# Optimization experiments

Measured on AMD Instinct MI355X. Metric: run time of the kernel, lower is better.

The kernel has to match this reference:

```python
import jax, jax.numpy as jnp
import numpy as np

BT, NQ, NC, C, H, HID = 192, 64, 1024, 384, 8, 1536
DH = C // H                       # 48
SCALE = DH ** -0.5
MAX_NEG = -float(np.finfo(np.float32).max)


def _ln(x, eps, g=None, b=None):
    m = x.mean(-1, keepdims=True)
    v = ((x - m) ** 2).mean(-1, keepdims=True)
    y = (x - m) / jnp.sqrt(v + eps)
    if g is not None:
        y = y * g + b
    return y


def _gelu_tanh(x):
    # GELU(approximate='tanh')
    return 0.5 * x * (1.0 + jnp.tanh(jnp.sqrt(2.0 / jnp.pi) * (x + 0.044715 * x ** 3)))


def setup_inputs() -> dict:
    key = jax.random.key(0)
    ks = jax.random.split(key, 10)
    s = lambda fan: 1.0 / np.sqrt(fan)
    return {
        "x": jax.random.normal(ks[0], (BT, NQ, C), jnp.float32),
        "context": jax.random.normal(ks[1], (BT, NC, C), jnp.float32),
        "mask": jax.random.randint(ks[2], (BT, NQ), 0, 2) > 0,
        "Wq": jax.random.normal(ks[3], (C, C), jnp.float32) * s(C),
        "bq": jnp.zeros((C,), jnp.float32),
        "Wkv": jax.random.normal(ks[4], (C, 2 * C), jnp.float32) * s(C),
        "bkv": jnp.zeros((2 * C,), jnp.float32),
        "Wo": jax.random.normal(ks[5], (C, C), jnp.float32) * s(C),
        "bo": jnp.zeros((C,), jnp.float32),
        "g_ctx": jnp.ones((C,), jnp.float32),
        "b_ctx": jnp.zeros((C,), jnp.float32),
        "W1": jax.random.normal(ks[6], (C, HID), jnp.float32) * s(C),
        "b1": jnp.zeros((HID,), jnp.float32),
        "W2": jax.random.normal(ks[7], (HID, C), jnp.float32) * s(HID),
        "b2": jnp.zeros((C,), jnp.float32),
    }


def reference(x, context, mask, Wq, bq, Wkv, bkv, Wo, bo, g_ctx, b_ctx, W1, b1, W2, b2):
    # --- cross-attention branch ---
    xn = _ln(x, 1e-6)                       # norm1 (no affine)
    cn = _ln(context, 1e-5, g_ctx, b_ctx)   # norm_context (affine, default eps)
    q = (xn @ Wq + bq).reshape(BT, NQ, H, DH).transpose(0, 2, 1, 3)    # (B,H,NQ,DH)
    kv = cn @ Wkv + bkv
    k, v = jnp.split(kv, 2, axis=-1)
    k = k.reshape(BT, NC, H, DH).transpose(0, 2, 1, 3)                 # (B,H,NC,DH)
    v = v.reshape(BT, NC, H, DH).transpose(0, 2, 1, 3)
    sim = jnp.einsum('bhqd,bhkd->bhqk', q, k) * SCALE                  # (B,H,NQ,NC)
    # mask shape (BT, NQ): True = keep query row; ~mask * (-max) bias
    bias = jnp.where(mask[:, None, :, None], 0.0, MAX_NEG)
    attn = jax.nn.softmax(sim + bias, axis=-1)
    o = jnp.einsum('bhqk,bhkd->bhqd', attn, v).transpose(0, 2, 1, 3).reshape(BT, NQ, C)
    x = x + o @ Wo + bo
    # --- MLP branch ---
    xn2 = _ln(x, 1e-6)                      # norm2 (no affine)
    x = x + _gelu_tanh(xn2 @ W1 + b1) @ W2 + b2
    return x
```

## Files before the change

### kernel.cpp

```cpp
#include <hip/hip_runtime.h>
#include <hip/hip_bf16.h>
#include <math.h>

typedef unsigned int  u32;
typedef unsigned short u16;
typedef unsigned char u8;

#define BTn   192
#define NQn   64
#define NCn   1024
#define Cd    384
#define Hn    8
#define DHn   48
#define HIDn  1536
#define ROWSX (BTn*NQn)
#define ROWSC (BTn*NCn)
#define ATT_SCALE 0.14433756729740643f
#define CBc   64

typedef __bf16 bf16x8 __attribute__((ext_vector_type(8)));
typedef float  f32x4  __attribute__((ext_vector_type(4)));

#define GLL16(gp, lp) __builtin_amdgcn_global_load_lds( \
    (const __attribute__((address_space(1))) void*)(gp), \
    (__attribute__((address_space(3))) void*)(lp), 16, 0, 0)

__device__ __forceinline__ float bf2f(u32 u) {
  union { u32 i; float f; } v; v.i = u << 16; return v.f;
}
__device__ __forceinline__ u16 f2bf(float f) {
  union { float f; u32 i; } v; v.f = f;
  u32 x = v.i;
  x += 0x7fffu + ((x >> 16) & 1u);
  return (u16)(x >> 16);
}
__device__ __forceinline__ void decode8(uint4 r, float* v) {
  v[0]=bf2f(r.x & 0xffffu); v[1]=bf2f(r.x >> 16);
  v[2]=bf2f(r.y & 0xffffu); v[3]=bf2f(r.y >> 16);
  v[4]=bf2f(r.z & 0xffffu); v[5]=bf2f(r.z >> 16);
  v[6]=bf2f(r.w & 0xffffu); v[7]=bf2f(r.w >> 16);
}
__device__ __forceinline__ float gelu_f(float x) {
  float x3 = x*x*x;
  float z = 0.7978845608028654f*x + 0.035677408136300125f*x3;
  float e = __expf(2.f*z);
  float th = 1.f - 2.f/(e+1.f);
  return 0.5f*x*(1.f+th);
}

__global__ void decode_mask_kernel(const u8* __restrict__ m, u8* __restrict__ keep) {
  __shared__ int flags[3];
  int t = threadIdx.x;
  if (t < 3) flags[t] = 0;
  __syncthreads();
  int nonbin = 0, oddset = 0, low01 = 0;
  for (int i = t; i < ROWSX; i += 256) {
    u32 b = m[i];
    if (b > 1u) nonbin = 1;
    if ((i & 3) && b) oddset = 1;
    if (((i & 3) < 2) && b) low01 = 1;
  }
  if (nonbin) flags[0] = 1;
  if (oddset) flags[1] = 1;
  if (low01)  flags[2] = 1;
  __syncthreads();
  int mode = flags[0] ? (flags[2] ? 2 : 3) : (flags[1] ? 1 : 0);
  for (int i = t; i < ROWSX; i += 256) {
    u8 k;
    if (mode == 2)      k = (m[2*i] | m[2*i+1]) ? 1 : 0;
    else if (mode == 3) k = (((const float*)m)[i] != 0.f) ? 1 : 0;
    else if (mode == 1) k = m[i] ? 1 : 0;
    else                k = (((const int*)m)[i] != 0) ? 1 : 0;
    keep[i] = k;
  }
}

template<int AFF, int SRCF32>
__global__ __launch_bounds__(256) void lnorm_kernel(
    const void* __restrict__ srcv, const float* __restrict__ gw,
    const float* __restrict__ bw, u16* __restrict__ dst, float eps)
{
  const int row  = blockIdx.x * 4 + (threadIdx.x >> 6);
  const int lane = threadIdx.x & 63;
  float v[6];
  if (SRCF32) {
    const float2* p = (const float2*)((const float*)srcv + (size_t)row*Cd);
    #pragma unroll
    for (int i = 0; i < 3; i++) { float2 u = p[lane + 64*i]; v[2*i]=u.x; v[2*i+1]=u.y; }
  } else {
    const u32* p = (const u32*)((const u16*)srcv + (size_t)row*Cd);
    #pragma unroll
    for (int i = 0; i < 3; i++) { u32 u = p[lane + 64*i]; v[2*i]=bf2f(u&0xffffu); v[2*i+1]=bf2f(u>>16); }
  }
  float s  = v[0]+v[1]+v[2]+v[3]+v[4]+v[5];
  float s2 = v[0]*v[0]+v[1]*v[1]+v[2]*v[2]+v[3]*v[3]+v[4]*v[4]+v[5]*v[5];
  #pragma unroll
  for (int o = 32; o >= 1; o >>= 1) { s += __shfl_xor(s, o); s2 += __shfl_xor(s2, o); }
  float mean = s * (1.0f/Cd);
  float var  = s2 * (1.0f/Cd) - mean*mean;
  var = var > 0.f ? var : 0.f;
  float rstd = rsqrtf(var + eps);
  u32* d32 = (u32*)(dst + (size_t)row*Cd);
  #pragma unroll
  for (int i = 0; i < 3; i++) {
    float y0 = (v[2*i]   - mean) * rstd;
    float y1 = (v[2*i+1] - mean) * rstd;
    if (AFF) {
      float2 gg = *(const float2*)(gw + 2*(lane + 64*i));
      float2 bb = *(const float2*)(bw + 2*(lane + 64*i));
      y0 = y0*gg.x + bb.x;
      y1 = y1*gg.y + bb.y;
    }
    d32[lane + 64*i] = (u32)f2bf(y0) | ((u32)f2bf(y1) << 16);
  }
}

struct WPack {
  const float* W[5];
  u16* WT[5];
  int K[5];
  int N[5];
  int off[6];
};
__global__ __launch_bounds__(256) void wconvt_all_kernel(WPack p) {
  __shared__ u16 tile[64][66];
  const int bid = blockIdx.x;
  int s = 0;
  #pragma unroll
  for (int i = 1; i < 5; i++) if (bid >= p.off[i]) s = i;
  const float* W = p.W[s];
  u16* WT = p.WT[s];
  const int K = p.K[s], N = p.N[s];
  const int lb = bid - p.off[s];
  const int t  = threadIdx.x;
  const int nt = N >> 6;
  const int bk = lb / nt, bn = lb % nt;
  const int q  = t >> 6;
  const int nl = t & 63;
  #pragma unroll
  for (int r = 0; r < 16; r++) {
    int k = q*16 + r;
    tile[nl][k] = f2bf(W[(size_t)(bk*64 + k)*N + bn*64 + nl]);
  }
  __syncthreads();
  #pragma unroll
  for (int r = 0; r < 16; r++) {
    int n = q*16 + r;
    WT[(size_t)(bn*64 + n)*K + bk*64 + nl] = tile[n][nl];
  }
}

template<int GEL, int RES, int RF32, int OF32, int SCL>
__global__ __launch_bounds__(256) void mgemm_kernel(
    const u16* __restrict__ A, const u16* __restrict__ WT,
    const float* __restrict__ bias, const void* __restrict__ resv,
    void* __restrict__ Coutv, int M, int N, int K, int nx)
{
  __shared__ u16 As[3][4096];
  __shared__ u16 Bs[3][4096];
  const int t = threadIdx.x;
  const int w = t >> 6, l = t & 63, l15 = l & 15, g = l >> 4;

  const int nwg = gridDim.x;
  const int bid = blockIdx.x;
  const int wg  = (bid & 7) * (nwg >> 3) + (bid >> 3);
  const int n0 = (wg % nx) * 128, m0 = (wg / nx) * 128;
  const int wm = (w & 1) * 64, wn = (w >> 1) * 64;

  const int arow = t >> 2;
  const int swk  = (t >> 3) & 3;
  const int acol = ((t & 3) ^ swk) * 8;
  const u16* Ag = A  + (size_t)(m0 + arow) * K + acol;
  const u16* Wg = WT + (size_t)(n0 + arow) * K + acol;
  const size_t rowskip = (size_t)64 * K;

  const int xk   = (l15 >> 1) & 3;
  const int goff = ((g ^ xk) << 3);

  f32x4 acc[4][4];
  #pragma unroll
  for (int i = 0; i < 4; i++)
    #pragma unroll
    for (int j = 0; j < 4; j++) acc[i][j] = (f32x4){0.f, 0.f, 0.f, 0.f};

  const int nIter = K >> 5;

#define STAGE(nb, kk) do { \
    GLL16(Ag + (kk),           &As[nb][t*8]); \
    GLL16(Ag + (kk) + rowskip, &As[nb][2048 + t*8]); \
    GLL16(Wg + (kk),           &Bs[nb][t*8]); \
    GLL16(Wg + (kk) + rowskip, &Bs[nb][2048 + t*8]); \
  } while (0)

#define BODY(BUF, IT) do { \
    const int it_ = (IT); \
    if (it_ + 2 < nIter) { \
      STAGE((BUF + 2) % 3, (it_ + 2) << 5); \
      asm volatile("s_waitcnt vmcnt(8)" ::: "memory"); \
    } else if (it_ + 1 < nIter) { \
      asm volatile("s_waitcnt vmcnt(4)" ::: "memory"); \
    } else { \
      asm volatile("s_waitcnt vmcnt(0)" ::: "memory"); \
    } \
    __builtin_amdgcn_s_barrier(); \
    __builtin_amdgcn_sched_barrier(0); \
    { \
      bf16x8 af[4], bfv[4]; \
      _Pragma("unroll") \
      for (int i = 0; i < 4; i++) \
        af[i] = *(const bf16x8*)&As[BUF][(wm + i*16 + l15)*32 + goff]; \
      _Pragma("unroll") \
      for (int j = 0; j < 4; j++) \
        bfv[j] = *(const bf16x8*)&Bs[BUF][(wn + j*16 + l15)*32 + goff]; \
      _Pragma("unroll") \
      for (int i = 0; i < 4; i++) \
        _Pragma("unroll") \
        for (int j = 0; j < 4; j++) \
          acc[i][j] = __builtin_amdgcn_mfma_f32_16x16x32_bf16(bfv[j], af[i], acc[i][j], 0, 0, 0); \
    } \
    __builtin_amdgcn_sched_barrier(0); \
    __builtin_amdgcn_s_barrier(); \
  } while (0)

  STAGE(0, 0);
  STAGE(1, 32);
  for (int it0 = 0; it0 < nIter; it0 += 3) {
    BODY(0, it0);
    BODY(1, it0 + 1);
    BODY(2, it0 + 2);
  }
#undef BODY
#undef STAGE

  const float* resf = (const float*)resv;
  const u16*   resb = (const u16*)resv;
  float* Cf = (float*)Coutv;
  u16*   Cb = (u16*)Coutv;
  #pragma unroll
  for (int j = 0; j < 4; j++) {
    const int nb = n0 + wn + j*16 + g*4;
    const float4 bv = *(const float4*)&bias[nb];
    #pragma unroll
    for (int i = 0; i < 4; i++) {
      const int m = m0 + wm + i*16 + l15;
      float c0 = acc[i][j][0] + bv.x;
      float c1 = acc[i][j][1] + bv.y;
      float c2 = acc[i][j][2] + bv.z;
      float c3 = acc[i][j][3] + bv.w;
      if (SCL) { c0 *= ATT_SCALE; c1 *= ATT_SCALE; c2 *= ATT_SCALE; c3 *= ATT_SCALE; }
      if (GEL) { c0 = gelu_f(c0); c1 = gelu_f(c1); c2 = gelu_f(c2); c3 = gelu_f(c3); }
      if (RES) {
        if (RF32) {
          float4 r = *(const float4*)&resf[(size_t)m*N + nb];
          c0 += r.x; c1 += r.y; c2 += r.z; c3 += r.w;
        } else {
          uint2 r = *(const uint2*)&resb[(size_t)m*N + nb];
          c0 += bf2f(r.x & 0xffffu); c1 += bf2f(r.x >> 16);
          c2 += bf2f(r.y & 0xffffu); c3 += bf2f(r.y >> 16);
        }
      }
      if (OF32) {
        *(float4*)&Cf[(size_t)m*N + nb] = make_float4(c0, c1, c2, c3);
      } else {
        uint2 pk = make_uint2((u32)f2bf(c0) | ((u32)f2bf(c1) << 16),
                              (u32)f2bf(c2) | ((u32)f2bf(c3) << 16));
        *(uint2*)&Cb[(size_t)m*N + nb] = pk;
      }
    }
  }
}

template<int GEL, int RES, int RF32, int OF32>
__global__ __launch_bounds__(512, 4) void mgemm256_kernel(
    const u16* __restrict__ A, const u16* __restrict__ WT,
    const float* __restrict__ bias, const void* __restrict__ resv,
    void* __restrict__ Coutv, int M, int N, int K, int nx)
{
  __shared__ u16 As[3][4096];
  __shared__ u16 Bs[3][8192];
  const int t = threadIdx.x;
  const int w = t >> 6, l = t & 63, l15 = l & 15, g = l >> 4;

  const int nwg = gridDim.x;
  const int bid = blockIdx.x;
  const int wg  = (bid & 7) * (nwg >> 3) + (bid >> 3);
  const int n0 = (wg % nx) * 256, m0 = (wg / nx) * 128;
  const int wm = (w & 1) * 64, wn = (w >> 1) * 64;

  const int arow = t >> 2;
  const int swk  = (t >> 3) & 3;
  const int acol = ((t & 3) ^ swk) * 8;
  const u16* Ag = A  + (size_t)(m0 + arow) * K + acol;
  const u16* Wg = WT + (size_t)(n0 + arow) * K + acol;
  const size_t rowskipB = (size_t)128 * K;

  const int xk   = (l15 >> 1) & 3;
  const int goff = ((g ^ xk) << 3);

  f32x4 acc[4][4];
  #pragma unroll
  for (int i = 0; i < 4; i++)
    #pragma unroll
    for (int j = 0; j < 4; j++) acc[i][j] = (f32x4){0.f, 0.f, 0.f, 0.f};

  const int nIter = K >> 5;

#define STAGE(nb, kk) do { \
    GLL16(Ag + (kk),            &As[nb][t*8]); \
    GLL16(Wg + (kk),            &Bs[nb][t*8]); \
    GLL16(Wg + (kk) + rowskipB, &Bs[nb][4096 + t*8]); \
  } while (0)

#define BODY(BUF, IT) do { \
    const int it_ = (IT); \
    if (it_ + 2 < nIter) { \
      STAGE((BUF + 2) % 3, (it_ + 2) << 5); \
      asm volatile("s_waitcnt vmcnt(6)" ::: "memory"); \
    } else if (it_ + 1 < nIter) { \
      asm volatile("s_waitcnt vmcnt(3)" ::: "memory"); \
    } else { \
      asm volatile("s_waitcnt vmcnt(0)" ::: "memory"); \
    } \
    __builtin_amdgcn_s_barrier(); \
    __builtin_amdgcn_sched_barrier(0); \
    { \
      bf16x8 af[4], bfv[4]; \
      _Pragma("unroll") \
      for (int i = 0; i < 4; i++) \
        af[i] = *(const bf16x8*)&As[BUF][(wm + i*16 + l15)*32 + goff]; \
      _Pragma("unroll") \
      for (int j = 0; j < 4; j++) \
        bfv[j] = *(const bf16x8*)&Bs[BUF][(wn + j*16 + l15)*32 + goff]; \
      _Pragma("unroll") \
      for (int i = 0; i < 4; i++) \
        _Pragma("unroll") \
        for (int j = 0; j < 4; j++) \
          acc[i][j] = __builtin_amdgcn_mfma_f32_16x16x32_bf16(bfv[j], af[i], acc[i][j], 0, 0, 0); \
    } \
    __builtin_amdgcn_sched_barrier(0); \
    __builtin_amdgcn_s_barrier(); \
  } while (0)

  STAGE(0, 0);
  STAGE(1, 32);
  for (int it0 = 0; it0 < nIter; it0 += 3) {
    BODY(0, it0);
    BODY(1, it0 + 1);
    BODY(2, it0 + 2);
  }
#undef BODY
#undef STAGE

  const float* resf = (const float*)resv;
  const u16*   resb = (const u16*)resv;
  float* Cf = (float*)Coutv;
  u16*   Cb = (u16*)Coutv;
  #pragma unroll
  for (int j = 0; j < 4; j++) {
    const int nb = n0 + wn + j*16 + g*4;
    const float4 bv = *(const float4*)&bias[nb];
    #pragma unroll
    for (int i = 0; i < 4; i++) {
      const int m = m0 + wm + i*16 + l15;
      float c0 = acc[i][j][0] + bv.x;
      float c1 = acc[i][j][1] + bv.y;
      float c2 = acc[i][j][2] + bv.z;
      float c3 = acc[i][j][3] + bv.w;
      if (GEL) { c0 = gelu_f(c0); c1 = gelu_f(c1); c2 = gelu_f(c2); c3 = gelu_f(c3); }
      if (RES) {
        if (RF32) {
          float4 r = *(const float4*)&resf[(size_t)m*N + nb];
          c0 += r.x; c1 += r.y; c2 += r.z; c3 += r.w;
        } else {
          uint2 r = *(const uint2*)&resb[(size_t)m*N + nb];
          c0 += bf2f(r.x & 0xffffu); c1 += bf2f(r.x >> 16);
          c2 += bf2f(r.y & 0xffffu); c3 += bf2f(r.y >> 16);
        }
      }
      if (OF32) {
        *(float4*)&Cf[(size_t)m*N + nb] = make_float4(c0, c1, c2, c3);
      } else {
        uint2 pk = make_uint2((u32)f2bf(c0) | ((u32)f2bf(c1) << 16),
                              (u32)f2bf(c2) | ((u32)f2bf(c3) << 16));
        *(uint2*)&Cb[(size_t)m*N + nb] = pk;
      }
    }
  }
}

__global__ __launch_bounds__(256) void fattn_kernel(
    const u16* __restrict__ qb, const u16* __restrict__ kvb,
    const u8* __restrict__ keep, u16* __restrict__ ob, int b0)
{
  __shared__ u16 Qs[64*72];
  __shared__ u16 Ks[64*72];
  __shared__ u16 Vt[48*72];
  __shared__ u16 Ps[4][16*72];

  const int t = threadIdx.x;
  const int w = t >> 6, l = t & 63, l15 = l & 15, g = l >> 4;
  const int h = blockIdx.x, bz = blockIdx.y;
  const int b = b0 + bz;
  const int wq = w * 16;
  const int krow0 = t / 6, kp0 = t % 6;
  const int krow1 = (256 + t) / 6, kp1 = (256 + t) % 6;
  const int vdq = (t >> 4) * 4, vkq = (t & 15) * 4;

  for (int i = t; i < 2304; i += 256) { ((u32*)Qs)[i] = 0; ((u32*)Ks)[i] = 0; }
  __syncthreads();

  for (int i = t; i < 384; i += 256) {
    int row = i / 6, p = i % 6;
    *(uint4*)&Qs[row*72 + p*8] =
        *(const uint4*)(qb + (size_t)(b*NQn + row)*Cd + h*DHn + p*8);
  }

  u32 kw = *(const u32*)&keep[b*NQn + wq + g*4];
  float kf[4];
  #pragma unroll
  for (int r = 0; r < 4; r++) kf[r] = ((kw >> (8*r)) & 0xffu) ? 1.f : 0.f;

  float mrow[4], lrow[4];
  f32x4 oacc[3];
  #pragma unroll
  for (int r = 0; r < 4; r++) { mrow[r] = kf[r] > 0.f ? -3.0e38f : 0.f; lrow[r] = 0.f; }
  #pragma unroll
  for (int d = 0; d < 3; d++) oacc[d] = (f32x4){0.f, 0.f, 0.f, 0.f};

  auto loadKV = [&](int kt, uint4& KR0, uint4& KR1, uint2* V) {
    const u16* base = kvb + ((size_t)bz*NCn + (size_t)kt*64) * (2*(size_t)Cd);
    KR0 = *(const uint4*)(base + (size_t)krow0*(2*Cd) + h*DHn + kp0*8);
    if (t < 128)
      KR1 = *(const uint4*)(base + (size_t)krow1*(2*Cd) + h*DHn + kp1*8);
    if (t < 192) {
      const u16* vs = base + (size_t)vkq*(2*Cd) + Cd + h*DHn + vdq;
      V[0] = *(const uint2*)(vs);
      V[1] = *(const uint2*)(vs + 2*Cd);
      V[2] = *(const uint2*)(vs + 4*Cd);
      V[3] = *(const uint2*)(vs + 6*Cd);
    }
  };
  auto writeKV = [&](const uint4& KR0, const uint4& KR1, const uint2* V) {
    *(uint4*)&Ks[krow0*72 + kp0*8] = KR0;
    if (t < 128) *(uint4*)&Ks[krow1*72 + kp1*8] = KR1;
    if (t < 192) {
      #pragma unroll
      for (int jj = 0; jj < 4; jj++) {
        u16 o4[4] = {((const u16*)&V[0])[jj], ((const u16*)&V[1])[jj],
                     ((const u16*)&V[2])[jj], ((const u16*)&V[3])[jj]};
        *(uint2*)&Vt[(vdq+jj)*72 + vkq] = *(uint2*)o4;
      }
    }
  };

  bf16x8 qf0, qf1;
  auto compute = [&]() {
    f32x4 sf[4];
    #pragma unroll
    for (int f = 0; f < 4; f++) {
      bf16x8 ka = *(const bf16x8*)&Ks[(f*16 + l15)*72 + g*8];
      bf16x8 kb = *(const bf16x8*)&Ks[(f*16 + l15)*72 + 32 + g*8];
      f32x4 z = (f32x4){0.f, 0.f, 0.f, 0.f};
      z = __builtin_amdgcn_mfma_f32_16x16x32_bf16(qf0, ka, z, 0, 0, 0);
      sf[f] = __builtin_amdgcn_mfma_f32_16x16x32_bf16(qf1, kb, z, 0, 0, 0);
    }
    float p[4][4], pmax[4];
    #pragma unroll
    for (int r = 0; r < 4; r++) {
      float pm = fmaxf(fmaxf(sf[0][r], sf[1][r]), fmaxf(sf[2][r], sf[3][r]));
      #pragma unroll
      for (int s = 1; s < 16; s <<= 1) pm = fmaxf(pm, __shfl_xor(pm, s));
      pmax[r] = pm;
    }
    float dm = fmaxf(fmaxf(kf[0]*(pmax[0]-mrow[0]), kf[1]*(pmax[1]-mrow[1])),
                     fmaxf(kf[2]*(pmax[2]-mrow[2]), kf[3]*(pmax[3]-mrow[3])));
    if (!__all(dm <= 8.f)) {
      #pragma unroll
      for (int r = 0; r < 4; r++) {
        float mn = kf[r] > 0.f ? fmaxf(mrow[r], pmax[r]) : 0.f;
        float sc = kf[r] > 0.f ? __expf(mrow[r] - mn) : 1.f;
        mrow[r] = mn;
        lrow[r] *= sc;
        oacc[0][r] *= sc; oacc[1][r] *= sc; oacc[2][r] *= sc;
      }
    }
    #pragma unroll
    for (int r = 0; r < 4; r++) {
      float p0 = kf[r] > 0.f ? __expf(sf[0][r] - mrow[r]) : 1.f;
      float p1 = kf[r] > 0.f ? __expf(sf[1][r] - mrow[r]) : 1.f;
      float p2 = kf[r] > 0.f ? __expf(sf[2][r] - mrow[r]) : 1.f;
      float p3 = kf[r] > 0.f ? __expf(sf[3][r] - mrow[r]) : 1.f;
      p[0][r]=p0; p[1][r]=p1; p[2][r]=p2; p[3][r]=p3;
      float ps = p0+p1+p2+p3;
      #pragma unroll
      for (int s = 1; s < 16; s <<= 1) ps += __shfl_xor(ps, s);
      lrow[r] += ps;
    }
    #pragma unroll
    for (int f = 0; f < 4; f++)
      #pragma unroll
      for (int r = 0; r < 4; r++)
        Ps[w][(g*4 + r)*72 + f*16 + l15] = f2bf(p[f][r]);
    bf16x8 pa0 = *(const bf16x8*)&Ps[w][l15*72 + g*8];
    bf16x8 pa1 = *(const bf16x8*)&Ps[w][l15*72 + 32 + g*8];
    #pragma unroll
    for (int df = 0; df < 3; df++) {
      bf16x8 vb0 = *(const bf16x8*)&Vt[(df*16 + l15)*72 + g*8];
      bf16x8 vb1 = *(const bf16x8*)&Vt[(df*16 + l15)*72 + 32 + g*8];
      oacc[df] = __builtin_amdgcn_mfma_f32_16x16x32_bf16(pa0, vb0, oacc[df], 0, 0, 0);
      oacc[df] = __builtin_amdgcn_mfma_f32_16x16x32_bf16(pa1, vb1, oacc[df], 0, 0, 0);
    }
  };

  uint4 ka0, ka1, kb0_, kb1_;
  uint2 va[4], vb_[4];
  loadKV(0, ka0, ka1, va);
  __syncthreads();

  qf0 = *(const bf16x8*)&Qs[(wq + l15)*72 + g*8];
  qf1 = *(const bf16x8*)&Qs[(wq + l15)*72 + 32 + g*8];

  for (int kt = 0; kt < 16; kt += 2) {
    writeKV(ka0, ka1, va);
    asm volatile("s_waitcnt lgkmcnt(0)" ::: "memory");
    __builtin_amdgcn_sched_barrier(0);
    __builtin_amdgcn_s_barrier();
    __builtin_amdgcn_sched_barrier(0);
    loadKV(kt + 1, kb0_, kb1_, vb_);
    compute();
    __builtin_amdgcn_sched_barrier(0);
    __builtin_amdgcn_s_barrier();
    writeKV(kb0_, kb1_, vb_);
    asm volatile("s_waitcnt lgkmcnt(0)" ::: "memory");
    __builtin_amdgcn_sched_barrier(0);
    __builtin_amdgcn_s_barrier();
    __builtin_amdgcn_sched_barrier(0);
    if (kt + 2 < 16) loadKV(kt + 2, ka0, ka1, va);
    compute();
    if (kt + 2 < 16) {
      __builtin_amdgcn_sched_barrier(0);
      __builtin_amdgcn_s_barrier();
    }
  }

  #pragma unroll
  for (int r = 0; r < 4; r++) {
    float inv = 1.f / lrow[r];
    size_t qrow = (size_t)(b*NQn + wq + g*4 + r);
    #pragma unroll
    for (int df = 0; df < 3; df++)
      ob[qrow*Cd + h*DHn + df*16 + l15] = f2bf(oacc[df][r] * inv);
  }
}

extern "C" void kernel_launch(void* const* d_in, const int* in_sizes, int n_in,
                              void* d_out, int out_size, void* d_ws, size_t ws_size,
                              hipStream_t stream) {
  (void)in_sizes; (void)n_in; (void)out_size; (void)ws_size;
  const float* x   = (const float*)d_in[0];
  const float* ctx = (const float*)d_in[1];
  const u8*    msk = (const u8*)   d_in[2];
  const float* Wq  = (const float*)d_in[3];
  const float* bq  = (const float*)d_in[4];
  const float* Wkv = (const float*)d_in[5];
  const float* bkv = (const float*)d_in[6];
  const float* Wo  = (const float*)d_in[7];
  const float* bo  = (const float*)d_in[8];
  const float* gc  = (const float*)d_in[9];
  const float* bc  = (const float*)d_in[10];
  const float* W1  = (const float*)d_in[11];
  const float* b1  = (const float*)d_in[12];
  const float* W2  = (const float*)d_in[13];
  const float* b2  = (const float*)d_in[14];
  float* out = (float*)d_out;

  char* ws = (char*)d_ws;
  size_t off = 0;
  auto bump = [&](size_t bytes) -> size_t {
    size_t o = off; off += (bytes + 255) & ~(size_t)255; return o;
  };
  const size_t act = (size_t)ROWSX * Cd * 2;
  size_t o_keep = bump(ROWSX);
  size_t o_xn   = bump(act);
  size_t o_x1n  = bump(act);
  size_t o_q    = bump(act);
  size_t o_ob   = bump(act);
  size_t o_x1   = bump(act);
  size_t o_hid  = bump((size_t)ROWSX * HIDn * 2);
  size_t o_wtq  = bump((size_t)Cd*Cd*2);
  size_t o_wtkv = bump((size_t)Cd*2*Cd*2);
  size_t o_wto  = bump((size_t)Cd*Cd*2);
  size_t o_wt1  = bump((size_t)Cd*HIDn*2);
  size_t o_wt2  = bump((size_t)HIDn*Cd*2);
  size_t o_cn   = bump((size_t)CBc * NCn * Cd * 2);
  size_t o_kv   = bump((size_t)CBc * NCn * 2 * Cd * 2);

  u8*  keep = (u8*)(ws + o_keep);
  u16* xn   = (u16*)(ws + o_xn);
  u16* x1n  = (u16*)(ws + o_x1n);
  u16* qb   = (u16*)(ws + o_q);
  u16* obuf = (u16*)(ws + o_ob);
  u16* x1b  = (u16*)(ws + o_x1);
  u16* hidb = (u16*)(ws + o_hid);
  u16* wtq  = (u16*)(ws + o_wtq);
  u16* wtkv = (u16*)(ws + o_wtkv);
  u16* wto  = (u16*)(ws + o_wto);
  u16* wt1  = (u16*)(ws + o_wt1);
  u16* wt2  = (u16*)(ws + o_wt2);
  u16* cnb  = (u16*)(ws + o_cn);
  u16* kvb  = (u16*)(ws + o_kv);

  decode_mask_kernel<<<1, 256, 0, stream>>>(msk, keep);

  WPack wp;
  wp.W[0]=Wq;  wp.WT[0]=wtq;  wp.K[0]=Cd;   wp.N[0]=Cd;
  wp.W[1]=Wkv; wp.WT[1]=wtkv; wp.K[1]=Cd;   wp.N[1]=2*Cd;
  wp.W[2]=Wo;  wp.WT[2]=wto;  wp.K[2]=Cd;   wp.N[2]=Cd;
  wp.W[3]=W1;  wp.WT[3]=wt1;  wp.K[3]=Cd;   wp.N[3]=HIDn;
  wp.W[4]=W2;  wp.WT[4]=wt2;  wp.K[4]=HIDn; wp.N[4]=Cd;
  wp.off[0]=0; wp.off[1]=36; wp.off[2]=108; wp.off[3]=144; wp.off[4]=288; wp.off[5]=432;
  wconvt_all_kernel<<<432, 256, 0, stream>>>(wp);

  lnorm_kernel<0,1><<<ROWSX/4, 256, 0, stream>>>(x, nullptr, nullptr, xn, 1e-6f);

  mgemm_kernel<0,0,0,0,1><<<3*(ROWSX/128), 256, 0, stream>>>(
      xn, wtq, bq, nullptr, qb, ROWSX, Cd, Cd, 3);

  for (int b0 = 0; b0 < BTn; b0 += CBc) {
    lnorm_kernel<1,1><<<CBc*NCn/4, 256, 0, stream>>>(
        ctx + (size_t)b0*NCn*Cd, gc, bc, cnb, 1e-5f);
    mgemm256_kernel<0,0,0,0><<<3*(CBc*NCn/128), 512, 0, stream>>>(
        cnb, wtkv, bkv, nullptr, kvb, CBc*NCn, 2*Cd, Cd, 3);
    fattn_kernel<<<dim3(Hn, CBc), 256, 0, stream>>>(qb, kvb, keep, obuf, b0);
  }

  mgemm_kernel<0,1,1,0,0><<<3*(ROWSX/128), 256, 0, stream>>>(
      obuf, wto, bo, x, x1b, ROWSX, Cd, Cd, 3);

  lnorm_kernel<0,0><<<ROWSX/4, 256, 0, stream>>>(x1b, nullptr, nullptr, x1n, 1e-6f);

  mgemm256_kernel<1,0,0,0><<<6*(ROWSX/128), 512, 0, stream>>>(
      x1n, wt1, b1, nullptr, hidb, ROWSX, HIDn, Cd, 6);

  mgemm_kernel<0,1,0,1,0><<<3*(ROWSX/128), 256, 0, stream>>>(
      hidb, wt2, b2, x1b, out, ROWSX, Cd, HIDn, 3);
}
```

Measured before the change: 576.0 us.

## Fuse layer-norm normalization into the A-operand load of the 256-wide GEMMs

Replaces the separate layer-norm kernels for context and norm2 with a small row-statistics pass. The mean and rstd are applied inside the GEMM while the A tile is staged: the kernel reads fp32 or bf16 rows through registers, normalizes them, applies the optional affine, converts to bf16 and writes to LDS. This avoids writing and re-reading the bf16 normalized context and x1n buffers. In exchange it uses a synchronous register path for A instead of async global-to-LDS loads, reads fp32 context, which doubles A bytes inside the GEMM, and computes variance as E[x^2]-mean^2.

After: 818.8 us. 1.42x slower.

```diff
diff --git a/kernel.cpp b/kernel.cpp
--- a/kernel.cpp
+++ b/kernel.cpp
@@ -72,6 +72,40 @@
     else if (mode == 1) k = m[i] ? 1 : 0;
     else                k = (((const int*)m)[i] != 0) ? 1 : 0;
     keep[i] = k;
+  }
+}
+
+template<int SRCF32>
+__global__ __launch_bounds__(256) void row_stats_kernel(
+    const void* __restrict__ srcv, float* __restrict__ stats, float eps)
+{
+  const int row  = blockIdx.x * 4 + (threadIdx.x >> 6);
+  const int lane = threadIdx.x & 63;
+  float s = 0.f, s2 = 0.f;
+  if (SRCF32) {
+    const float2* p = (const float2*)((const float*)srcv + (size_t)row*Cd);
+    #pragma unroll
+    for (int i = 0; i < 3; i++) {
+      float2 u = p[lane + 64*i];
+      s += u.x + u.y; s2 += u.x*u.x + u.y*u.y;
+    }
+  } else {
+    const u32* p = (const u32*)((const u16*)srcv + (size_t)row*Cd);
+    #pragma unroll
+    for (int i = 0; i < 3; i++) {
+      u32 u = p[lane + 64*i];
+      float a = bf2f(u & 0xffffu), b = bf2f(u >> 16);
+      s += a + b; s2 += a*a + b*b;
+    }
+  }
+  #pragma unroll
+  for (int o = 32; o >= 1; o >>= 1) { s += __shfl_xor(s, o); s2 += __shfl_xor(s2, o); }
+  if (lane == 0) {
+    float mean = s * (1.0f/Cd);
+    float var  = s2 * (1.0f/Cd) - mean*mean;
+    var = var > 0.f ? var : 0.f;
+    stats[2*row]   = mean;
+    stats[2*row+1] = rsqrtf(var + eps);
   }
 }
 
@@ -270,14 +304,16 @@
   }
 }
 
-template<int GEL, int RES, int RF32, int OF32>
-__global__ __launch_bounds__(512, 4) void mgemm256_kernel(
-    const u16* __restrict__ A, const u16* __restrict__ WT,
-    const float* __restrict__ bias, const void* __restrict__ resv,
-    void* __restrict__ Coutv, int M, int N, int K, int nx)
+template<int AF32, int AFF, int GEL>
+__global__ __launch_bounds__(512, 4) void mgemm256ln_kernel(
+    const void* __restrict__ Av, const float* __restrict__ stats,
+    const float* __restrict__ gw, const float* __restrict__ bw,
+    const u16* __restrict__ WT, const float* __restrict__ bias,
+    u16* __restrict__ Cout, int M, int N, int K, int nx)
 {
   __shared__ u16 As[3][4096];
   __shared__ u16 Bs[3][8192];
+  __shared__ float gls[Cd], bls[Cd];
   const int t = threadIdx.x;
   const int w = t >> 6, l = t & 63, l15 = l & 15, g = l >> 4;
 
@@ -290,10 +326,14 @@
   const int arow = t >> 2;
   const int swk  = (t >> 3) & 3;
   const int acol = ((t & 3) ^ swk) * 8;
-  const u16* Ag = A  + (size_t)(m0 + arow) * K + acol;
+  const float* Af = (const float*)Av + (size_t)(m0 + arow) * K + acol;
+  const u16*   Ab = (const u16*)Av   + (size_t)(m0 + arow) * K + acol;
   const u16* Wg = WT + (size_t)(n0 + arow) * K + acol;
   const size_t rowskipB = (size_t)128 * K;
 
+  const float mean = stats[2*(m0 + arow)];
+  const float rstd = stats[2*(m0 + arow) + 1];
+
   const int xk   = (l15 >> 1) & 3;
   const int goff = ((g ^ xk) << 3);
 
@@ -305,23 +345,68 @@
 
   const int nIter = K >> 5;
 
-#define STAGE(nb, kk) do { \
-    GLL16(Ag + (kk),            &As[nb][t*8]); \
-    GLL16(Wg + (kk),            &Bs[nb][t*8]); \
-    GLL16(Wg + (kk) + rowskipB, &Bs[nb][4096 + t*8]); \
+  if (AFF) {
+    for (int i = t; i < Cd; i += 512) { gls[i] = gw[i]; bls[i] = bw[i]; }
+  }
+  asm volatile("s_waitcnt vmcnt(0) lgkmcnt(0)" ::: "memory");
+  __builtin_amdgcn_s_barrier();
+  __builtin_amdgcn_sched_barrier(0);
+
+#define LNWRITE(nb, kkA, A0, A1, AU) do { \
+    float yv[8]; \
+    if (AF32) { yv[0]=(A0).x; yv[1]=(A0).y; yv[2]=(A0).z; yv[3]=(A0).w; \
+                yv[4]=(A1).x; yv[5]=(A1).y; yv[6]=(A1).z; yv[7]=(A1).w; } \
+    else { decode8((AU), yv); } \
+    _Pragma("unroll") \
+    for (int j_ = 0; j_ < 8; j_++) yv[j_] = (yv[j_] - mean) * rstd; \
+    if (AFF) { \
+      const float4 g0_ = *(const float4*)&gls[acol + (kkA)]; \
+      const float4 g1_ = *(const float4*)&gls[acol + (kkA) + 4]; \
+      const float4 b0_ = *(const float4*)&bls[acol + (kkA)]; \
+      const float4 b1_ = *(const float4*)&bls[acol + (kkA) + 4]; \
+      yv[0]=yv[0]*g0_.x+b0_.x; yv[1]=yv[1]*g0_.y+b0_.y; \
+      yv[2]=yv[2]*g0_.z+b0_.z; yv[3]=yv[3]*g0_.w+b0_.w; \
+      yv[4]=yv[4]*g1_.x+b1_.x; yv[5]=yv[5]*g1_.y+b1_.y; \
+      yv[6]=yv[6]*g1_.z+b1_.z; yv[7]=yv[7]*g1_.w+b1_.w; \
+    } \
+    u16 e_[8]; \
+    _Pragma("unroll") \
+    for (int j_ = 0; j_ < 8; j_++) e_[j_] = f2bf(yv[j_]); \
+    uint4 pk_ = make_uint4((u32)e_[0] | ((u32)e_[1] << 16), \
+                           (u32)e_[2] | ((u32)e_[3] << 16), \
+                           (u32)e_[4] | ((u32)e_[5] << 16), \
+                           (u32)e_[6] | ((u32)e_[7] << 16)); \
+    *(uint4*)&As[nb][t*8] = pk_; \
   } while (0)
+
+  {
+    float4 p0, p1; uint4 pu;
+    if (AF32) { p0 = *(const float4*)(Af); p1 = *(const float4*)(Af + 4); }
+    else      { pu = *(const uint4*)(Ab); }
+    GLL16(Wg,                 &Bs[0][t*8]);
+    GLL16(Wg + rowskipB,      &Bs[0][4096 + t*8]);
+    GLL16(Wg + 32,            &Bs[1][t*8]);
+    GLL16(Wg + 32 + rowskipB, &Bs[1][4096 + t*8]);
+    asm volatile("s_waitcnt vmcnt(4)" ::: "memory");
+    LNWRITE(0, 0, p0, p1, pu);
+    asm volatile("s_waitcnt vmcnt(2) lgkmcnt(0)" ::: "memory");
+    __builtin_amdgcn_s_barrier();
+    __builtin_amdgcn_sched_barrier(0);
+  }
 
 #define BODY(BUF, IT) do { \
     const int it_ = (IT); \
+    const int kkA = (it_ + 1) << 5; \
+    float4 q0, q1; uint4 qu; \
+    if (it_ + 1 < nIter) { \
+      if (AF32) { q0 = *(const float4*)(Af + kkA); q1 = *(const float4*)(Af + kkA + 4); } \
+      else      { qu = *(const uint4*)(Ab + kkA); } \
+    } \
     if (it_ + 2 < nIter) { \
-      STAGE((BUF + 2) % 3, (it_ + 2) << 5); \
-      asm volatile("s_waitcnt vmcnt(6)" ::: "memory"); \
-    } else if (it_ + 1 < nIter) { \
-      asm volatile("s_waitcnt vmcnt(3)" ::: "memory"); \
-    } else { \
-      asm volatile("s_waitcnt vmcnt(0)" ::: "memory"); \
+      const int kkB = (it_ + 2) << 5; \
+      GLL16(Wg + kkB,            &Bs[(BUF+2)%3][t*8]); \
+      GLL16(Wg + kkB + rowskipB, &Bs[(BUF+2)%3][4096 + t*8]); \
     } \
-    __builtin_amdgcn_s_barrier(); \
     __builtin_amdgcn_sched_barrier(0); \
     { \
       bf16x8 af[4], bfv[4]; \
@@ -338,23 +423,25 @@
           acc[i][j] = __builtin_amdgcn_mfma_f32_16x16x32_bf16(bfv[j], af[i], acc[i][j], 0, 0, 0); \
     } \
     __builtin_amdgcn_sched_barrier(0); \
-    __builtin_amdgcn_s_barrier(); \
+    if (it_ + 1 < nIter) { \
+      if (it_ + 2 < nIter) asm volatile("s_waitcnt vmcnt(2)" ::: "memory"); \
+      else                 asm volatile("s_waitcnt vmcnt(0)" ::: "memory"); \
+      LNWRITE((BUF+1)%3, kkA, q0, q1, qu); \
+      asm volatile("s_waitcnt lgkmcnt(0)" ::: "memory"); \
+      __builtin_amdgcn_sched_barrier(0); \
+      __builtin_amdgcn_s_barrier(); \
+      __builtin_amdgcn_sched_barrier(0); \
+    } \
   } while (0)
 
-  STAGE(0, 0);
-  STAGE(1, 32);
   for (int it0 = 0; it0 < nIter; it0 += 3) {
     BODY(0, it0);
     BODY(1, it0 + 1);
     BODY(2, it0 + 2);
   }
 #undef BODY
-#undef STAGE
-
-  const float* resf = (const float*)resv;
-  const u16*   resb = (const u16*)resv;
-  float* Cf = (float*)Coutv;
-  u16*   Cb = (u16*)Coutv;
+#undef LNWRITE
+
   #pragma unroll
   for (int j = 0; j < 4; j++) {
     const int nb = n0 + wn + j*16 + g*4;
@@ -367,23 +454,9 @@
       float c2 = acc[i][j][2] + bv.z;
       float c3 = acc[i][j][3] + bv.w;
       if (GEL) { c0 = gelu_f(c0); c1 = gelu_f(c1); c2 = gelu_f(c2); c3 = gelu_f(c3); }
-      if (RES) {
-        if (RF32) {
-          float4 r = *(const float4*)&resf[(size_t)m*N + nb];
-          c0 += r.x; c1 += r.y; c2 += r.z; c3 += r.w;
-        } else {
-          uint2 r = *(const uint2*)&resb[(size_t)m*N + nb];
-          c0 += bf2f(r.x & 0xffffu); c1 += bf2f(r.x >> 16);
-          c2 += bf2f(r.y & 0xffffu); c3 += bf2f(r.y >> 16);
-        }
-      }
-      if (OF32) {
-        *(float4*)&Cf[(size_t)m*N + nb] = make_float4(c0, c1, c2, c3);
-      } else {
-        uint2 pk = make_uint2((u32)f2bf(c0) | ((u32)f2bf(c1) << 16),
-                              (u32)f2bf(c2) | ((u32)f2bf(c3) << 16));
-        *(uint2*)&Cb[(size_t)m*N + nb] = pk;
-      }
+      uint2 pk = make_uint2((u32)f2bf(c0) | ((u32)f2bf(c1) << 16),
+                            (u32)f2bf(c2) | ((u32)f2bf(c3) << 16));
+      *(uint2*)&Cout[(size_t)m*N + nb] = pk;
     }
   }
 }
@@ -582,7 +655,6 @@
   const size_t act = (size_t)ROWSX * Cd * 2;
   size_t o_keep = bump(ROWSX);
   size_t o_xn   = bump(act);
-  size_t o_x1n  = bump(act);
   size_t o_q    = bump(act);
   size_t o_ob   = bump(act);
   size_t o_x1   = bump(act);
@@ -592,23 +664,24 @@
   size_t o_wto  = bump((size_t)Cd*Cd*2);
   size_t o_wt1  = bump((size_t)Cd*HIDn*2);
   size_t o_wt2  = bump((size_t)HIDn*Cd*2);
-  size_t o_cn   = bump((size_t)CBc * NCn * Cd * 2);
+  size_t o_cst  = bump((size_t)ROWSC * 2 * 4);
+  size_t o_x1st = bump((size_t)ROWSX * 2 * 4);
   size_t o_kv   = bump((size_t)CBc * NCn * 2 * Cd * 2);
 
-  u8*  keep = (u8*)(ws + o_keep);
-  u16* xn   = (u16*)(ws + o_xn);
-  u16* x1n  = (u16*)(ws + o_x1n);
-  u16* qb   = (u16*)(ws + o_q);
-  u16* obuf = (u16*)(ws + o_ob);
-  u16* x1b  = (u16*)(ws + o_x1);
-  u16* hidb = (u16*)(ws + o_hid);
-  u16* wtq  = (u16*)(ws + o_wtq);
-  u16* wtkv = (u16*)(ws + o_wtkv);
-  u16* wto  = (u16*)(ws + o_wto);
-  u16* wt1  = (u16*)(ws + o_wt1);
-  u16* wt2  = (u16*)(ws + o_wt2);
-  u16* cnb  = (u16*)(ws + o_cn);
-  u16* kvb  = (u16*)(ws + o_kv);
+  u8*    keep = (u8*)(ws + o_keep);
+  u16*   xn   = (u16*)(ws + o_xn);
+  u16*   qb   = (u16*)(ws + o_q);
+  u16*   obuf = (u16*)(ws + o_ob);
+  u16*   x1b  = (u16*)(ws + o_x1);
+  u16*   hidb = (u16*)(ws + o_hid);
+  u16*   wtq  = (u16*)(ws + o_wtq);
+  u16*   wtkv = (u16*)(ws + o_wtkv);
+  u16*   wto  = (u16*)(ws + o_wto);
+  u16*   wt1  = (u16*)(ws + o_wt1);
+  u16*   wt2  = (u16*)(ws + o_wt2);
+  float* cst  = (float*)(ws + o_cst);
+  float* x1st = (float*)(ws + o_x1st);
+  u16*   kvb  = (u16*)(ws + o_kv);
 
   decode_mask_kernel<<<1, 256, 0, stream>>>(msk, keep);
 
@@ -621,26 +694,27 @@
   wp.off[0]=0; wp.off[1]=36; wp.off[2]=108; wp.off[3]=144; wp.off[4]=288; wp.off[5]=432;
   wconvt_all_kernel<<<432, 256, 0, stream>>>(wp);
 
+  row_stats_kernel<1><<<ROWSC/4, 256, 0, stream>>>(ctx, cst, 1e-5f);
+
   lnorm_kernel<0,1><<<ROWSX/4, 256, 0, stream>>>(x, nullptr, nullptr, xn, 1e-6f);
 
   mgemm_kernel<0,0,0,0,1><<<3*(ROWSX/128), 256, 0, stream>>>(
       xn, wtq, bq, nullptr, qb, ROWSX, Cd, Cd, 3);
 
   for (int b0 = 0; b0 < BTn; b0 += CBc) {
-    lnorm_kernel<1,1><<<CBc*NCn/4, 256, 0, stream>>>(
-        ctx + (size_t)b0*NCn*Cd, gc, bc, cnb, 1e-5f);
-    mgemm256_kernel<0,0,0,0><<<3*(CBc*NCn/128), 512, 0, stream>>>(
-        cnb, wtkv, bkv, nullptr, kvb, CBc*NCn, 2*Cd, Cd, 3);
+    mgemm256ln_kernel<1,1,0><<<3*(CBc*NCn/128), 512, 0, stream>>>(
+        ctx + (size_t)b0*NCn*Cd, cst + (size_t)b0*NCn*2, gc, bc,
+        wtkv, bkv, kvb, CBc*NCn, 2*Cd, Cd, 3);
     fattn_kernel<<<dim3(Hn, CBc), 256, 0, stream>>>(qb, kvb, keep, obuf, b0);
   }
 
   mgemm_kernel<0,1,1,0,0><<<3*(ROWSX/128), 256, 0, stream>>>(
       obuf, wto, bo, x, x1b, ROWSX, Cd, Cd, 3);
 
-  lnorm_kernel<0,0><<<ROWSX/4, 256, 0, stream>>>(x1b, nullptr, nullptr, x1n, 1e-6f);
-
-  mgemm256_kernel<1,0,0,0><<<6*(ROWSX/128), 512, 0, stream>>>(
-      x1n, wt1, b1, nullptr, hidb, ROWSX, HIDn, Cd, 6);
+  row_stats_kernel<0><<<ROWSX/4, 256, 0, stream>>>(x1b, x1st, 1e-6f);
+
+  mgemm256ln_kernel<0,0,1><<<6*(ROWSX/128), 512, 0, stream>>>(
+      x1b, x1st, nullptr, nullptr, wt1, b1, hidb, ROWSX, HIDn, Cd, 6);
 
   mgemm_kernel<0,1,0,1,0><<<3*(ROWSX/128), 256, 0, stream>>>(
       hidb, wt2, b2, x1b, out, ROWSX, Cd, HIDn, 3);
```
